# Kernel tuning notes

Measured on AMD Instinct MI355X. Metric: run time of the kernel, lower is better.

The kernel has to match this reference:

```python
import jax, jax.numpy as jnp
import numpy as np

N_LAYERS = 2
D_MODEL = 1024
D_INNER = 2 * D_MODEL
D_STATE = 16
D_CONV = 4
DT_RANK = D_MODEL // 16  # 64
B_SZ, L = 1, 2048
EPS = 1e-5


def layernorm(x, w, b):
    mu = jnp.mean(x, axis=-1, keepdims=True)
    var = jnp.mean(jnp.square(x - mu), axis=-1, keepdims=True)
    return (x - mu) * jax.lax.rsqrt(var + EPS) * w + b


def mamba(x, in_w, cw, cb, xp_w, dtp_w, dtp_b, A_log, Dp, out_w):
    # x: [B, L, D_MODEL]
    Bn, Ln, _ = x.shape
    xz = jnp.einsum('bld,ed->ble', x, in_w)          # [B,L,2*D_INNER]
    xc, z = jnp.split(xz, 2, axis=-1)
    # causal depthwise conv1d (kernel D_CONV)
    xp = jnp.pad(xc, ((0, 0), (D_CONV - 1, 0), (0, 0)))
    xc = sum(xp[:, k:k + Ln, :] * cw[:, k] for k in range(D_CONV)) + cb
    xc = jax.nn.silu(xc)
    dbl = jnp.einsum('ble,re->blr', xc, xp_w)        # [B,L,DT_RANK+2*D_STATE]
    dt, Bm, Cm = jnp.split(dbl, [DT_RANK, DT_RANK + D_STATE], axis=-1)
    dt = jax.nn.softplus(jnp.einsum('blr,er->ble', dt, dtp_w) + dtp_b)  # [B,L,E]
    A = -jnp.exp(A_log)                              # [E,N], strictly negative
    dA = jnp.exp(dt[..., None] * A)                  # [B,L,E,N]
    dBu = (dt * xc)[..., None] * Bm[:, :, None, :]   # [B,L,E,N]

    def step(h, inp):
        dA_t, dBu_t, C_t = inp
        h = dA_t * h + dBu_t                         # [B,E,N]
        y = jnp.einsum('ben,bn->be', h, C_t)
        return h, y

    h0 = jnp.zeros((Bn, D_INNER, D_STATE), dA.dtype)
    _, ys = jax.lax.scan(step, h0, (dA.transpose(1, 0, 2, 3),
                                    dBu.transpose(1, 0, 2, 3),
                                    Cm.transpose(1, 0, 2)))
    y = ys.transpose(1, 0, 2) + xc * Dp              # [B,L,E]
    y = y * jax.nn.silu(z)
    return jnp.einsum('ble,de->bld', y, out_w)       # [B,L,D_MODEL]


def setup_inputs() -> dict:
    key = jax.random.key(0)
    ks = jax.random.split(key, 12)
    s = 0.02
    dt_init = np.log(np.expm1(0.01)).astype(np.float32)  # softplus^-1(0.01)
    A_row = jnp.log(jnp.arange(1, D_STATE + 1, dtype=jnp.float32))
    return {
        'x': jax.random.normal(ks[0], (B_SZ, L, D_MODEL), jnp.float32),
        'ln_w': jnp.ones((N_LAYERS, D_MODEL), jnp.float32),
        'ln_b': jnp.zeros((N_LAYERS, D_MODEL), jnp.float32),
        'in_proj_w': jax.random.normal(ks[1], (N_LAYERS, 2 * D_INNER, D_MODEL)) * s,
        'conv_w': jax.random.normal(ks[2], (N_LAYERS, D_INNER, D_CONV)) * 0.2,
        'conv_b': jnp.zeros((N_LAYERS, D_INNER), jnp.float32),
        'x_proj_w': jax.random.normal(ks[3], (N_LAYERS, DT_RANK + 2 * D_STATE, D_INNER)) * s,
        'dt_proj_w': jax.random.normal(ks[4], (N_LAYERS, D_INNER, DT_RANK)) * (DT_RANK ** -0.5),
        'dt_proj_b': jnp.full((N_LAYERS, D_INNER), dt_init),
        'A_log': jnp.broadcast_to(A_row, (N_LAYERS, D_INNER, D_STATE)).copy(),
        'D_skip': jnp.ones((N_LAYERS, D_INNER), jnp.float32),
        'out_proj_w': jax.random.normal(ks[5], (N_LAYERS, D_MODEL, D_INNER)) * s,
        'norm_f_w': jnp.ones((D_MODEL,), jnp.float32),
        'norm_f_b': jnp.zeros((D_MODEL,), jnp.float32),
    }


def reference(x, ln_w, ln_b, in_proj_w, conv_w, conv_b, x_proj_w, dt_proj_w,
              dt_proj_b, A_log, D_skip, out_proj_w, norm_f_w, norm_f_b):
    for i in range(N_LAYERS):
        h = layernorm(x, ln_w[i], ln_b[i])
        h = mamba(h, in_proj_w[i], conv_w[i], conv_b[i], x_proj_w[i],
                  dt_proj_w[i], dt_proj_b[i], A_log[i], D_skip[i], out_proj_w[i])
        x = h + x  # residual (dropout/drop_path are identity in eval)
    return layernorm(x, norm_f_w, norm_f_b)
```

## Files before the change

### kernel.cpp

```cpp
#include <hip/hip_runtime.h>
#include <hip/hip_bf16.h>
#include <math.h>

#define LSEQ 2048
#define DMODEL 1024
#define DINNER 2048
#define DSTATE 16
#define DCONV 4
#define DTRANK 64
#define RPROJ 96

#define CHUNK 16
#define NCHUNK (LSEQ / CHUNK)

#define XSPLIT 4

typedef __attribute__((ext_vector_type(8))) short bf16x8;
typedef __attribute__((ext_vector_type(4))) float f32x4;

__device__ __forceinline__ float softplusf(float x) {
    return (x > 20.f) ? x : log1pf(__expf(x));
}
__device__ __forceinline__ float siluf(float x) {
    return x / (1.f + __expf(-x));
}
__device__ __forceinline__ short f2bf(float f) {
    union { float f; unsigned u; } v; v.f = f;
    unsigned r = v.u + 0x7FFFu + ((v.u >> 16) & 1u);
    return (short)(r >> 16);
}
__device__ __forceinline__ float bf2f(short h) {
    union { unsigned u; float f; } v;
    v.u = ((unsigned)(unsigned short)h) << 16;
    return v.f;
}

__device__ __forceinline__ void cvt8(const float* __restrict__ s,
                                     short* __restrict__ d, int i) {
    const float4 a = *(const float4*)(s + i);
    const float4 b = *(const float4*)(s + i + 4);
    alignas(16) short h[8];
    h[0] = f2bf(a.x); h[1] = f2bf(a.y); h[2] = f2bf(a.z); h[3] = f2bf(a.w);
    h[4] = f2bf(b.x); h[5] = f2bf(b.y); h[6] = f2bf(b.z); h[7] = f2bf(b.w);
    *(uint4*)(d + i) = *(const uint4*)h;
}

__global__ __launch_bounds__(256) void cvt_weights(
    const float* __restrict__ s0, short* __restrict__ d0, int n0,
    const float* __restrict__ s1, short* __restrict__ d1, int n1,
    const float* __restrict__ s2, short* __restrict__ d2, int n2,
    const float* __restrict__ s3, short* __restrict__ d3, int n3)
{
    int i = (blockIdx.x * 256 + threadIdx.x) * 8;
    if (i < n0) { cvt8(s0, d0, i); return; }
    i -= n0;
    if (i < n1) { cvt8(s1, d1, i); return; }
    i -= n1;
    if (i < n2) { cvt8(s2, d2, i); return; }
    i -= n2;
    if (i < n3) { cvt8(s3, d3, i); return; }
}

__global__ __launch_bounds__(256) void ln_kernel(
    const float* __restrict__ x, const float* __restrict__ w,
    const float* __restrict__ b, float* __restrict__ outf,
    short* __restrict__ outb)
{
    __shared__ float s1[256], s2[256];
    const int row = blockIdx.x;
    const int tid = threadIdx.x;
    const float* xr = x + (size_t)row * DMODEL;
    float v[4];
    float s = 0.f, sq = 0.f;
#pragma unroll
    for (int k = 0; k < 4; k++) {
        v[k] = xr[k * 256 + tid];
        s += v[k];
        sq += v[k] * v[k];
    }
    s1[tid] = s; s2[tid] = sq;
    __syncthreads();
    for (int off = 128; off > 0; off >>= 1) {
        if (tid < off) { s1[tid] += s1[tid + off]; s2[tid] += s2[tid + off]; }
        __syncthreads();
    }
    const float mu = s1[0] * (1.f / DMODEL);
    const float var = s2[0] * (1.f / DMODEL) - mu * mu;
    const float rstd = rsqrtf(var + 1e-5f);
#pragma unroll
    for (int k = 0; k < 4; k++) {
        const int i = k * 256 + tid;
        const float o = (v[k] - mu) * rstd * w[i] + b[i];
        if (outf) outf[(size_t)row * DMODEL + i] = o;
        if (outb) outb[(size_t)row * DMODEL + i] = f2bf(o);
    }
}

template<int MI, int NJ, int MODE>
__global__ __launch_bounds__(256) void gemm_mfma(
    const short* __restrict__ A, int lda,
    const short* __restrict__ W, int ldw,
    float* __restrict__ Cf, short* __restrict__ Cb, int ldc,
    int M, int N, int K,
    const float* __restrict__ bias,
    const float* __restrict__ resid,
    size_t csplit)
{
    constexpr int BM = 32 * MI;
    constexpr int BN = 32 * NJ;
    constexpr int AISS = BM / 64;
    constexpr int WISS = BN / 64;
    __shared__ alignas(16) short As[2][BM * 32];
    __shared__ alignas(16) short Ws[2][BN * 32];

    const int tid = threadIdx.x;
    const int lane = tid & 63;
    const int w = tid >> 6;
    const int wr = w >> 1, wc = w & 1;
    const int row0 = blockIdx.y * BM;
    const int col0 = blockIdx.x * BN;
    const int kbeg = blockIdx.z * K;

    const int srow = tid >> 2;
    const int skch = ((tid & 3) ^ ((srow >> 1) & 3)) * 8;

    f32x4 acc[MI][NJ];
#pragma unroll
    for (int i = 0; i < MI; i++)
#pragma unroll
        for (int j = 0; j < NJ; j++) acc[i][j] = (f32x4)0.f;

    const int lrow = lane & 15;
    const int q = lane >> 4;
    const int NIT = K / 32;

    auto stage = [&](int p, int kt) {
#pragma unroll
        for (int j = 0; j < AISS; j++) {
            const short* gp = A + (size_t)(row0 + j * 64 + srow) * lda + kt + skch;
            __builtin_amdgcn_global_load_lds(
                (const __attribute__((address_space(1))) void*)gp,
                (__attribute__((address_space(3))) void*)(&As[p][j * 2048 + tid * 8]),
                16, 0, 0);
        }
#pragma unroll
        for (int j = 0; j < WISS; j++) {
            const int wrow = col0 + j * 64 + srow;
            if (wrow < N) {
                const short* gp = W + (size_t)wrow * ldw + kt + skch;
                __builtin_amdgcn_global_load_lds(
                    (const __attribute__((address_space(1))) void*)gp,
                    (__attribute__((address_space(3))) void*)(&Ws[p][j * 2048 + tid * 8]),
                    16, 0, 0);
            }
        }
    };

    stage(0, kbeg);
    __syncthreads();
    for (int it = 0; it < NIT; ++it) {
        const int p = it & 1;
        if (it + 1 < NIT) stage(p ^ 1, kbeg + (it + 1) * 32);

        bf16x8 af[MI], bfr[NJ];
#pragma unroll
        for (int i = 0; i < MI; i++) {
            const int R = wr * (16 * MI) + i * 16 + lrow;
            af[i] = *(const bf16x8*)&As[p][R * 32 + ((q ^ ((R >> 1) & 3)) * 8)];
        }
#pragma unroll
        for (int j = 0; j < NJ; j++) {
            const int R = wc * (16 * NJ) + j * 16 + lrow;
            bfr[j] = *(const bf16x8*)&Ws[p][R * 32 + ((q ^ ((R >> 1) & 3)) * 8)];
        }
#pragma unroll
        for (int i = 0; i < MI; i++)
#pragma unroll
            for (int j = 0; j < NJ; j++)
                acc[i][j] = __builtin_amdgcn_mfma_f32_16x16x32_bf16(
                    af[i], bfr[j], acc[i][j], 0, 0, 0);
        __syncthreads();
    }

    if (MODE == 0 && csplit) Cf += blockIdx.z * csplit;

    const int rbase = row0 + wr * (16 * MI);
    const int cbase = col0 + wc * (16 * NJ);
#pragma unroll
    for (int i = 0; i < MI; i++) {
#pragma unroll
        for (int j = 0; j < NJ; j++) {
            const int gcol = cbase + j * 16 + lrow;
            if (gcol < N) {
#pragma unroll
                for (int r = 0; r < 4; r++) {
                    const int grow = rbase + i * 16 + (lane >> 4) * 4 + r;
                    float v = acc[i][j][r];
                    if (MODE == 2) v += resid[(size_t)grow * ldc + gcol];
                    if (MODE == 5) v = softplusf(v + bias[gcol]);
                    if (MODE == 3 || MODE == 5) {
                        Cb[(size_t)grow * ldc + gcol] = f2bf(v);
                    } else {
                        Cf[(size_t)grow * ldc + gcol] = v;
                    }
                }
            }
        }
    }
}

__global__ __launch_bounds__(256) void combine_xproj(
    const float* __restrict__ part,
    float* __restrict__ dbl, short* __restrict__ dblb)
{
    const int i = (blockIdx.x * 256 + threadIdx.x) * 4;
    const int S = LSEQ * RPROJ;
    float4 v = *(const float4*)(part + i);
#pragma unroll
    for (int s = 1; s < XSPLIT; s++) {
        const float4 p = *(const float4*)(part + s * S + i);
        v.x += p.x; v.y += p.y; v.z += p.z; v.w += p.w;
    }
    *(float4*)(dbl + i) = v;
    alignas(8) short h[4] = {f2bf(v.x), f2bf(v.y), f2bf(v.z), f2bf(v.w)};
    *(unsigned long long*)(dblb + i) = *(const unsigned long long*)h;
}

__global__ __launch_bounds__(256) void conv_silu_kernel(
    const short* __restrict__ xzb, const float* __restrict__ cw,
    const float* __restrict__ cb, short* __restrict__ xcb)
{
    const int g = blockIdx.x * 256 + threadIdx.x;
    const int t = g >> 8;
    const int c0 = (g & 255) * 8;
    float acc[8];
#pragma unroll
    for (int j = 0; j < 8; j++) acc[j] = cb[c0 + j];
#pragma unroll
    for (int k = 0; k < DCONV; k++) {
        const int tt = t - (DCONV - 1) + k;
        if (tt >= 0) {
            const bf16x8 v = *(const bf16x8*)(xzb + (size_t)tt * (2 * DINNER) + c0);
#pragma unroll
            for (int j = 0; j < 8; j++)
                acc[j] += bf2f(v[j]) * cw[(c0 + j) * DCONV + k];
        }
    }
    alignas(16) short h[8];
#pragma unroll
    for (int j = 0; j < 8; j++) h[j] = f2bf(siluf(acc[j]));
    *(uint4*)(xcb + (size_t)t * DINNER + c0) = *(const uint4*)h;
}

__global__ __launch_bounds__(256) void scan_pass1(
    const short* __restrict__ dtb,
    const short* __restrict__ xcb,
    const float* __restrict__ dbl,
    const float* __restrict__ A_log,
    float* __restrict__ S,
    float* __restrict__ sumdt)
{
    const int e = blockIdx.x * 256 + threadIdx.x;
    const int c = blockIdx.y;
    float a[DSTATE];
#pragma unroll
    for (int n = 0; n < DSTATE; n++) a[n] = -__expf(A_log[(size_t)e * DSTATE + n]);
    float h[DSTATE];
#pragma unroll
    for (int n = 0; n < DSTATE; n++) h[n] = 0.f;
    float sd = 0.f;

    __shared__ float sBC[CHUNK][32];
    for (int i = threadIdx.x; i < CHUNK * 32; i += 256) {
        const int tl = i >> 5, j = i & 31;
        sBC[tl][j] = dbl[(size_t)(c * CHUNK + tl) * RPROJ + DTRANK + j];
    }
    __syncthreads();

    const size_t rb = (size_t)c * CHUNK * DINNER + e;
    short dt_c = dtb[rb], xc_c = xcb[rb];
#pragma unroll
    for (int tl = 0; tl < CHUNK; tl++) {
        short dt_n = 0, xc_n = 0;
        if (tl + 1 < CHUNK) {
            dt_n = dtb[rb + (size_t)(tl + 1) * DINNER];
            xc_n = xcb[rb + (size_t)(tl + 1) * DINNER];
        }
        const float dtv = bf2f(dt_c);
        const float du = dtv * bf2f(xc_c);
        sd += dtv;
#pragma unroll
        for (int n = 0; n < DSTATE; n++) {
            const float dA = __expf(dtv * a[n]);
            h[n] = dA * h[n] + du * sBC[tl][n];
        }
        dt_c = dt_n; xc_c = xc_n;
    }
    sumdt[(size_t)c * DINNER + e] = sd;
#pragma unroll
    for (int n = 0; n < DSTATE; n++)
        S[((size_t)c * DSTATE + n) * DINNER + e] = h[n];
}

__global__ __launch_bounds__(256) void scan_pass2(
    const float* __restrict__ A_log,
    const float* __restrict__ sumdt,
    float* __restrict__ S)
{
    const int idx = blockIdx.x * 256 + threadIdx.x;
    const int e = idx & (DINNER - 1);
    const int n = idx >> 11;
    const float a = -__expf(A_log[(size_t)e * DSTATE + n]);
    const size_t base = (size_t)n * DINNER + e;
    const size_t cstr = (size_t)DSTATE * DINNER;
    float H = 0.f;
    float sc = S[base];
    float sd = sumdt[e];
    for (int c = 0; c < NCHUNK; c++) {
        float sc_n = 0.f, sd_n = 0.f;
        if (c + 1 < NCHUNK) {
            sc_n = S[base + (size_t)(c + 1) * cstr];
            sd_n = sumdt[(size_t)(c + 1) * DINNER + e];
        }
        S[base + (size_t)c * cstr] = H;
        H = __expf(a * sd) * H + sc;
        sc = sc_n; sd = sd_n;
    }
}

__global__ __launch_bounds__(256) void scan_pass3(
    const short* __restrict__ dtb,
    const short* __restrict__ xcb,
    const float* __restrict__ dbl,
    const short* __restrict__ xzb,
    const float* __restrict__ A_log,
    const float* __restrict__ Dp,
    const float* __restrict__ S,
    short* __restrict__ yb)
{
    const int e = blockIdx.x * 256 + threadIdx.x;
    const int c = blockIdx.y;
    float a[DSTATE];
#pragma unroll
    for (int n = 0; n < DSTATE; n++) a[n] = -__expf(A_log[(size_t)e * DSTATE + n]);
    float h[DSTATE];
#pragma unroll
    for (int n = 0; n < DSTATE; n++)
        h[n] = S[((size_t)c * DSTATE + n) * DINNER + e];
    const float dskip = Dp[e];

    __shared__ float sBC[CHUNK][32];
    for (int i = threadIdx.x; i < CHUNK * 32; i += 256) {
        const int tl = i >> 5, j = i & 31;
        sBC[tl][j] = dbl[(size_t)(c * CHUNK + tl) * RPROJ + DTRANK + j];
    }
    __syncthreads();

    const size_t rb = (size_t)c * CHUNK * DINNER + e;
    const size_t zb = (size_t)c * CHUNK * (2 * DINNER) + DINNER + e;
    short dt_c = dtb[rb], xc_c = xcb[rb], z_c = xzb[zb];
#pragma unroll
    for (int tl = 0; tl < CHUNK; tl++) {
        short dt_n = 0, xc_n = 0, z_n = 0;
        if (tl + 1 < CHUNK) {
            dt_n = dtb[rb + (size_t)(tl + 1) * DINNER];
            xc_n = xcb[rb + (size_t)(tl + 1) * DINNER];
            z_n = xzb[zb + (size_t)(tl + 1) * (2 * DINNER)];
        }
        const float dtv = bf2f(dt_c);
        const float xcv = bf2f(xc_c);
        const float du = dtv * xcv;
        float yv = 0.f;
#pragma unroll
        for (int n = 0; n < DSTATE; n++) {
            const float dA = __expf(dtv * a[n]);
            h[n] = dA * h[n] + du * sBC[tl][n];
            yv += h[n] * sBC[tl][16 + n];
        }
        yv = (yv + xcv * dskip) * siluf(bf2f(z_c));
        yb[rb + (size_t)tl * DINNER] = f2bf(yv);
        dt_c = dt_n; xc_c = xc_n; z_c = z_n;
    }
}

extern "C" void kernel_launch(void* const* d_in, const int* in_sizes, int n_in,
                              void* d_out, int out_size, void* d_ws, size_t ws_size,
                              hipStream_t stream) {
    const float* x_in   = (const float*)d_in[0];
    const float* ln_w   = (const float*)d_in[1];
    const float* ln_b   = (const float*)d_in[2];
    const float* in_w   = (const float*)d_in[3];
    const float* conv_w = (const float*)d_in[4];
    const float* conv_b = (const float*)d_in[5];
    const float* xp_w   = (const float*)d_in[6];
    const float* dtp_w  = (const float*)d_in[7];
    const float* dtp_b  = (const float*)d_in[8];
    const float* A_log  = (const float*)d_in[9];
    const float* D_skip = (const float*)d_in[10];
    const float* out_w  = (const float*)d_in[11];
    const float* nf_w   = (const float*)d_in[12];
    const float* nf_b   = (const float*)d_in[13];
    float* out = (float*)d_out;

    float* w = (float*)d_ws;
    float* buf_x = w; w += (size_t)LSEQ * DMODEL;
    float* dbl   = w; w += (size_t)LSEQ * RPROJ;
    float* xpart = w; w += (size_t)XSPLIT * LSEQ * RPROJ;
    float* Sbuf  = w; w += (size_t)NCHUNK * DSTATE * DINNER;
    float* sumdt = w; w += (size_t)NCHUNK * DINNER;
    short* h_bf    = (short*)w; w += (size_t)LSEQ * DMODEL / 2;
    short* xz_bf   = (short*)w; w += (size_t)LSEQ * 2 * DINNER / 2;
    short* xc_bf   = (short*)w; w += (size_t)LSEQ * DINNER / 2;
    short* dt_bf   = (short*)w; w += (size_t)LSEQ * DINNER / 2;
    short* y_bf    = (short*)w; w += (size_t)LSEQ * DINNER / 2;
    short* dbl_bf  = (short*)w; w += (size_t)LSEQ * RPROJ / 2 + 1;
    short* in_w_bf  = (short*)w; w += (size_t)2 * (2 * DINNER) * DMODEL / 2;
    short* xp_w_bf  = (short*)w; w += (size_t)2 * RPROJ * DINNER / 2;
    short* dtp_w_bf = (short*)w; w += (size_t)2 * DINNER * DTRANK / 2;
    short* out_w_bf = (short*)w; w += (size_t)2 * DMODEL * DINNER / 2;

    {
        const int n1 = 2 * (2 * DINNER) * DMODEL;
        const int n2 = 2 * RPROJ * DINNER;
        const int n3 = 2 * DMODEL * DINNER;
        const int n4 = 2 * DINNER * DTRANK;
        const int total = n1 + n2 + n3 + n4;
        cvt_weights<<<dim3(total / (256 * 8)), dim3(256), 0, stream>>>(
            in_w, in_w_bf, n1, xp_w, xp_w_bf, n2,
            out_w, out_w_bf, n3, dtp_w, dtp_w_bf, n4);
    }

    for (int layer = 0; layer < 2; layer++) {
        const float* resid_src = (layer == 0) ? x_in : buf_x;
        ln_kernel<<<dim3(LSEQ), dim3(256), 0, stream>>>(
            resid_src, ln_w + layer * DMODEL, ln_b + layer * DMODEL,
            nullptr, h_bf);
        gemm_mfma<2, 4, 3><<<dim3((2 * DINNER) / 128, LSEQ / 64), dim3(256), 0, stream>>>(
            h_bf, DMODEL, in_w_bf + (size_t)layer * 2 * DINNER * DMODEL, DMODEL,
            nullptr, xz_bf, 2 * DINNER, LSEQ, 2 * DINNER, DMODEL, nullptr, nullptr, 0);
        conv_silu_kernel<<<dim3((LSEQ * DINNER / 8) / 256), dim3(256), 0, stream>>>(
            xz_bf, conv_w + (size_t)layer * DINNER * DCONV, conv_b + layer * DINNER,
            xc_bf);
        gemm_mfma<2, 2, 0><<<dim3(2, LSEQ / 64, XSPLIT), dim3(256), 0, stream>>>(
            xc_bf, DINNER, xp_w_bf + (size_t)layer * RPROJ * DINNER, DINNER,
            xpart, nullptr, RPROJ, LSEQ, RPROJ, DINNER / XSPLIT, nullptr, nullptr,
            (size_t)LSEQ * RPROJ);
        combine_xproj<<<dim3((LSEQ * RPROJ / 4) / 256), dim3(256), 0, stream>>>(
            xpart, dbl, dbl_bf);
        gemm_mfma<2, 4, 5><<<dim3(DINNER / 128, LSEQ / 64), dim3(256), 0, stream>>>(
            dbl_bf, RPROJ, dtp_w_bf + (size_t)layer * DINNER * DTRANK, DTRANK,
            nullptr, dt_bf, DINNER, LSEQ, DINNER, DTRANK,
            dtp_b + layer * DINNER, nullptr, 0);
        const float* Al = A_log + (size_t)layer * DINNER * DSTATE;
        scan_pass1<<<dim3(DINNER / 256, NCHUNK), dim3(256), 0, stream>>>(
            dt_bf, xc_bf, dbl, Al, Sbuf, sumdt);
        scan_pass2<<<dim3((DINNER * DSTATE) / 256), dim3(256), 0, stream>>>(
            Al, sumdt, Sbuf);
        scan_pass3<<<dim3(DINNER / 256, NCHUNK), dim3(256), 0, stream>>>(
            dt_bf, xc_bf, dbl, xz_bf, Al, D_skip + layer * DINNER, Sbuf, y_bf);
        gemm_mfma<2, 2, 2><<<dim3(DMODEL / 64, LSEQ / 64), dim3(256), 0, stream>>>(
            y_bf, DINNER, out_w_bf + (size_t)layer * DMODEL * DINNER, DINNER,
            buf_x, nullptr, DMODEL, LSEQ, DMODEL, DINNER, nullptr, resid_src, 0);
    }
    ln_kernel<<<dim3(LSEQ), dim3(256), 0, stream>>>(buf_x, nf_w, nf_b, out, nullptr);
}
```

Before: 496.8 us.

## Single-buffer GEMM, atomic split-K for x_proj, dedicated dt_proj kernel, bigger in_proj tile

Replaces the double-buffered LDS pipeline in the generic MFMA GEMM with a single buffer and two barriers per K step. The x_proj split-K partials are now accumulated with atomicAdd into dbl, which conv_silu zeroes, so the combine kernel and the partial buffer go away. A new dt_proj kernel converts fp32 dbl to bf16 on load and applies bias plus softplus. The in_proj GEMM moves to a 128x128 tile. Dropping double buffering exposes global load latency, and float atomics make the summation order nondeterministic.

After: 458.8 us. 7.6% less time.

```diff
diff --git a/kernel.cpp b/kernel.cpp
--- a/kernel.cpp
+++ b/kernel.cpp
@@ -102,16 +102,14 @@
     const short* __restrict__ W, int ldw,
     float* __restrict__ Cf, short* __restrict__ Cb, int ldc,
     int M, int N, int K,
-    const float* __restrict__ bias,
-    const float* __restrict__ resid,
-    size_t csplit)
+    const float* __restrict__ resid)
 {
     constexpr int BM = 32 * MI;
     constexpr int BN = 32 * NJ;
     constexpr int AISS = BM / 64;
     constexpr int WISS = BN / 64;
-    __shared__ alignas(16) short As[2][BM * 32];
-    __shared__ alignas(16) short Ws[2][BN * 32];
+    __shared__ alignas(16) short As[BM * 32];
+    __shared__ alignas(16) short Ws[BN * 32];
 
     const int tid = threadIdx.x;
     const int lane = tid & 63;
@@ -132,15 +130,15 @@
 
     const int lrow = lane & 15;
     const int q = lane >> 4;
-    const int NIT = K / 32;
-
-    auto stage = [&](int p, int kt) {
+
+    for (int kt = kbeg; kt < kbeg + K; kt += 32) {
+        __syncthreads();
 #pragma unroll
         for (int j = 0; j < AISS; j++) {
             const short* gp = A + (size_t)(row0 + j * 64 + srow) * lda + kt + skch;
             __builtin_amdgcn_global_load_lds(
                 (const __attribute__((address_space(1))) void*)gp,
-                (__attribute__((address_space(3))) void*)(&As[p][j * 2048 + tid * 8]),
+                (__attribute__((address_space(3))) void*)(&As[j * 2048 + tid * 8]),
                 16, 0, 0);
         }
 #pragma unroll
@@ -150,28 +148,22 @@
                 const short* gp = W + (size_t)wrow * ldw + kt + skch;
                 __builtin_amdgcn_global_load_lds(
                     (const __attribute__((address_space(1))) void*)gp,
-                    (__attribute__((address_space(3))) void*)(&Ws[p][j * 2048 + tid * 8]),
+                    (__attribute__((address_space(3))) void*)(&Ws[j * 2048 + tid * 8]),
                     16, 0, 0);
             }
         }
-    };
-
-    stage(0, kbeg);
-    __syncthreads();
-    for (int it = 0; it < NIT; ++it) {
-        const int p = it & 1;
-        if (it + 1 < NIT) stage(p ^ 1, kbeg + (it + 1) * 32);
+        __syncthreads();
 
         bf16x8 af[MI], bfr[NJ];
 #pragma unroll
         for (int i = 0; i < MI; i++) {
             const int R = wr * (16 * MI) + i * 16 + lrow;
-            af[i] = *(const bf16x8*)&As[p][R * 32 + ((q ^ ((R >> 1) & 3)) * 8)];
+            af[i] = *(const bf16x8*)&As[R * 32 + ((q ^ ((R >> 1) & 3)) * 8)];
         }
 #pragma unroll
         for (int j = 0; j < NJ; j++) {
             const int R = wc * (16 * NJ) + j * 16 + lrow;
-            bfr[j] = *(const bf16x8*)&Ws[p][R * 32 + ((q ^ ((R >> 1) & 3)) * 8)];
+            bfr[j] = *(const bf16x8*)&Ws[R * 32 + ((q ^ ((R >> 1) & 3)) * 8)];
         }
 #pragma unroll
         for (int i = 0; i < MI; i++)
@@ -179,10 +171,7 @@
             for (int j = 0; j < NJ; j++)
                 acc[i][j] = __builtin_amdgcn_mfma_f32_16x16x32_bf16(
                     af[i], bfr[j], acc[i][j], 0, 0, 0);
-        __syncthreads();
-    }
-
-    if (MODE == 0 && csplit) Cf += blockIdx.z * csplit;
+    }
 
     const int rbase = row0 + wr * (16 * MI);
     const int cbase = col0 + wc * (16 * NJ);
@@ -196,12 +185,13 @@
                 for (int r = 0; r < 4; r++) {
                     const int grow = rbase + i * 16 + (lane >> 4) * 4 + r;
                     float v = acc[i][j][r];
-                    if (MODE == 2) v += resid[(size_t)grow * ldc + gcol];
-                    if (MODE == 5) v = softplusf(v + bias[gcol]);
-                    if (MODE == 3 || MODE == 5) {
+                    if (MODE == 2) {
+                        Cf[(size_t)grow * ldc + gcol] =
+                            v + resid[(size_t)grow * ldc + gcol];
+                    } else if (MODE == 3) {
                         Cb[(size_t)grow * ldc + gcol] = f2bf(v);
                     } else {
-                        Cf[(size_t)grow * ldc + gcol] = v;
+                        atomicAdd(&Cf[(size_t)grow * ldc + gcol], v);
                     }
                 }
             }
@@ -209,28 +199,96 @@
     }
 }
 
-__global__ __launch_bounds__(256) void combine_xproj(
-    const float* __restrict__ part,
-    float* __restrict__ dbl, short* __restrict__ dblb)
-{
-    const int i = (blockIdx.x * 256 + threadIdx.x) * 4;
-    const int S = LSEQ * RPROJ;
-    float4 v = *(const float4*)(part + i);
-#pragma unroll
-    for (int s = 1; s < XSPLIT; s++) {
-        const float4 p = *(const float4*)(part + s * S + i);
-        v.x += p.x; v.y += p.y; v.z += p.z; v.w += p.w;
-    }
-    *(float4*)(dbl + i) = v;
-    alignas(8) short h[4] = {f2bf(v.x), f2bf(v.y), f2bf(v.z), f2bf(v.w)};
-    *(unsigned long long*)(dblb + i) = *(const unsigned long long*)h;
+__global__ __launch_bounds__(256) void dtproj_kernel(
+    const float* __restrict__ dbl,
+    const short* __restrict__ dtp_w,
+    const float* __restrict__ dtp_b,
+    short* __restrict__ dt_bf)
+{
+    __shared__ alignas(16) short As[64 * 32];
+    __shared__ alignas(16) short Ws[128 * 32];
+    const int tid = threadIdx.x;
+    const int lane = tid & 63;
+    const int w = tid >> 6;
+    const int wr = w >> 1, wc = w & 1;
+    const int row0 = blockIdx.y * 64;
+    const int col0 = blockIdx.x * 128;
+    const int srow = tid >> 2;
+    const int skch = ((tid & 3) ^ ((srow >> 1) & 3)) * 8;
+    const int lrow = lane & 15;
+    const int q = lane >> 4;
+
+    f32x4 acc[2][4];
+#pragma unroll
+    for (int i = 0; i < 2; i++)
+#pragma unroll
+        for (int j = 0; j < 4; j++) acc[i][j] = (f32x4)0.f;
+
+#pragma unroll
+    for (int kt = 0; kt < 64; kt += 32) {
+        __syncthreads();
+        {
+            const float* gp = dbl + (size_t)(row0 + srow) * RPROJ + kt + skch;
+            const float4 a = *(const float4*)gp;
+            const float4 b = *(const float4*)(gp + 4);
+            alignas(16) short h[8];
+            h[0] = f2bf(a.x); h[1] = f2bf(a.y); h[2] = f2bf(a.z); h[3] = f2bf(a.w);
+            h[4] = f2bf(b.x); h[5] = f2bf(b.y); h[6] = f2bf(b.z); h[7] = f2bf(b.w);
+            *(uint4*)(As + tid * 8) = *(const uint4*)h;
+        }
+#pragma unroll
+        for (int j = 0; j < 2; j++) {
+            const short* gp = dtp_w + (size_t)(col0 + j * 64 + srow) * DTRANK + kt + skch;
+            __builtin_amdgcn_global_load_lds(
+                (const __attribute__((address_space(1))) void*)gp,
+                (__attribute__((address_space(3))) void*)(&Ws[j * 2048 + tid * 8]),
+                16, 0, 0);
+        }
+        __syncthreads();
+
+        bf16x8 af[2], bfr[4];
+#pragma unroll
+        for (int i = 0; i < 2; i++) {
+            const int R = wr * 32 + i * 16 + lrow;
+            af[i] = *(const bf16x8*)&As[R * 32 + ((q ^ ((R >> 1) & 3)) * 8)];
+        }
+#pragma unroll
+        for (int j = 0; j < 4; j++) {
+            const int R = wc * 64 + j * 16 + lrow;
+            bfr[j] = *(const bf16x8*)&Ws[R * 32 + ((q ^ ((R >> 1) & 3)) * 8)];
+        }
+#pragma unroll
+        for (int i = 0; i < 2; i++)
+#pragma unroll
+            for (int j = 0; j < 4; j++)
+                acc[i][j] = __builtin_amdgcn_mfma_f32_16x16x32_bf16(
+                    af[i], bfr[j], acc[i][j], 0, 0, 0);
+    }
+
+    const int rbase = row0 + wr * 32;
+    const int cbase = col0 + wc * 64;
+#pragma unroll
+    for (int i = 0; i < 2; i++)
+#pragma unroll
+        for (int j = 0; j < 4; j++) {
+            const int gcol = cbase + j * 16 + lrow;
+#pragma unroll
+            for (int r = 0; r < 4; r++) {
+                const int grow = rbase + i * 16 + (lane >> 4) * 4 + r;
+                dt_bf[(size_t)grow * DINNER + gcol] =
+                    f2bf(softplusf(acc[i][j][r] + dtp_b[gcol]));
+            }
+        }
 }
 
 __global__ __launch_bounds__(256) void conv_silu_kernel(
     const short* __restrict__ xzb, const float* __restrict__ cw,
-    const float* __restrict__ cb, short* __restrict__ xcb)
+    const float* __restrict__ cb, short* __restrict__ xcb,
+    float* __restrict__ dbl_zero)
 {
     const int g = blockIdx.x * 256 + threadIdx.x;
+    if (g < (LSEQ * RPROJ) / 4)
+        *(float4*)(dbl_zero + g * 4) = make_float4(0.f, 0.f, 0.f, 0.f);
     const int t = g >> 8;
     const int c0 = (g & 255) * 8;
     float acc[8];
@@ -405,7 +463,6 @@
     float* w = (float*)d_ws;
     float* buf_x = w; w += (size_t)LSEQ * DMODEL;
     float* dbl   = w; w += (size_t)LSEQ * RPROJ;
-    float* xpart = w; w += (size_t)XSPLIT * LSEQ * RPROJ;
     float* Sbuf  = w; w += (size_t)NCHUNK * DSTATE * DINNER;
     float* sumdt = w; w += (size_t)NCHUNK * DINNER;
     short* h_bf    = (short*)w; w += (size_t)LSEQ * DMODEL / 2;
@@ -413,7 +470,6 @@
     short* xc_bf   = (short*)w; w += (size_t)LSEQ * DINNER / 2;
     short* dt_bf   = (short*)w; w += (size_t)LSEQ * DINNER / 2;
     short* y_bf    = (short*)w; w += (size_t)LSEQ * DINNER / 2;
-    short* dbl_bf  = (short*)w; w += (size_t)LSEQ * RPROJ / 2 + 1;
     short* in_w_bf  = (short*)w; w += (size_t)2 * (2 * DINNER) * DMODEL / 2;
     short* xp_w_bf  = (short*)w; w += (size_t)2 * RPROJ * DINNER / 2;
     short* dtp_w_bf = (short*)w; w += (size_t)2 * DINNER * DTRANK / 2;
@@ -435,22 +491,18 @@
         ln_kernel<<<dim3(LSEQ), dim3(256), 0, stream>>>(
             resid_src, ln_w + layer * DMODEL, ln_b + layer * DMODEL,
             nullptr, h_bf);
-        gemm_mfma<2, 4, 3><<<dim3((2 * DINNER) / 128, LSEQ / 64), dim3(256), 0, stream>>>(
+        gemm_mfma<4, 4, 3><<<dim3((2 * DINNER) / 128, LSEQ / 128), dim3(256), 0, stream>>>(
             h_bf, DMODEL, in_w_bf + (size_t)layer * 2 * DINNER * DMODEL, DMODEL,
-            nullptr, xz_bf, 2 * DINNER, LSEQ, 2 * DINNER, DMODEL, nullptr, nullptr, 0);
+            nullptr, xz_bf, 2 * DINNER, LSEQ, 2 * DINNER, DMODEL, nullptr);
         conv_silu_kernel<<<dim3((LSEQ * DINNER / 8) / 256), dim3(256), 0, stream>>>(
             xz_bf, conv_w + (size_t)layer * DINNER * DCONV, conv_b + layer * DINNER,
-            xc_bf);
-        gemm_mfma<2, 2, 0><<<dim3(2, LSEQ / 64, XSPLIT), dim3(256), 0, stream>>>(
+            xc_bf, dbl);
+        gemm_mfma<2, 2, 6><<<dim3(2, LSEQ / 64, XSPLIT), dim3(256), 0, stream>>>(
             xc_bf, DINNER, xp_w_bf + (size_t)layer * RPROJ * DINNER, DINNER,
-            xpart, nullptr, RPROJ, LSEQ, RPROJ, DINNER / XSPLIT, nullptr, nullptr,
-            (size_t)LSEQ * RPROJ);
-        combine_xproj<<<dim3((LSEQ * RPROJ / 4) / 256), dim3(256), 0, stream>>>(
-            xpart, dbl, dbl_bf);
-        gemm_mfma<2, 4, 5><<<dim3(DINNER / 128, LSEQ / 64), dim3(256), 0, stream>>>(
-            dbl_bf, RPROJ, dtp_w_bf + (size_t)layer * DINNER * DTRANK, DTRANK,
-            nullptr, dt_bf, DINNER, LSEQ, DINNER, DTRANK,
-            dtp_b + layer * DINNER, nullptr, 0);
+            dbl, nullptr, RPROJ, LSEQ, RPROJ, DINNER / XSPLIT, nullptr);
+        dtproj_kernel<<<dim3(DINNER / 128, LSEQ / 64), dim3(256), 0, stream>>>(
+            dbl, dtp_w_bf + (size_t)layer * DINNER * DTRANK,
+            dtp_b + layer * DINNER, dt_bf);
         const float* Al = A_log + (size_t)layer * DINNER * DSTATE;
         scan_pass1<<<dim3(DINNER / 256, NCHUNK), dim3(256), 0, stream>>>(
             dt_bf, xc_bf, dbl, Al, Sbuf, sumdt);
@@ -460,7 +512,7 @@
             dt_bf, xc_bf, dbl, xz_bf, Al, D_skip + layer * DINNER, Sbuf, y_bf);
         gemm_mfma<2, 2, 2><<<dim3(DMODEL / 64, LSEQ / 64), dim3(256), 0, stream>>>(
             y_bf, DINNER, out_w_bf + (size_t)layer * DMODEL * DINNER, DINNER,
-            buf_x, nullptr, DMODEL, LSEQ, DMODEL, DINNER, nullptr, resid_src, 0);
+            buf_x, nullptr, DMODEL, LSEQ, DMODEL, DINNER, resid_src);
     }
     ln_kernel<<<dim3(LSEQ), dim3(256), 0, stream>>>(buf_x, nf_w, nf_b, out, nullptr);
 }
```
